# Performance work log

Measured on AMD Instinct MI355X. Metric: run time of the kernel, lower is better.

Reference implementation:

```python
import jax, jax.numpy as jnp
import numpy as np

EPS = 1e-5
DN = ('NCDHW', 'OIDHW', 'NCDHW')

def conv3d(x, w, b):
    y = jax.lax.conv_general_dilated(x, w, (1, 1, 1), 'SAME', dimension_numbers=DN)
    return y + b[None, :, None, None, None]

def batchnorm(x, gamma, beta):
    # training-mode BatchNorm3d: biased batch stats over (N, D, H, W) per channel
    mean = jnp.mean(x, axis=(0, 2, 3, 4), keepdims=True)
    var = jnp.mean((x - mean) ** 2, axis=(0, 2, 3, 4), keepdims=True)
    xhat = (x - mean) * jax.lax.rsqrt(var + EPS)
    return gamma[None, :, None, None, None] * xhat + beta[None, :, None, None, None]

def setup_inputs() -> dict:
    key = jax.random.key(0)
    ks = jax.random.split(key, 8)
    C, N = 32, 4  # channel, fuzzynum
    B, D, H, W = 4, 64, 64, 64
    x = jax.random.normal(ks[0], (B, C, D, H, W), dtype=jnp.float32)
    fan1 = C * 27
    conv1_w = jax.random.uniform(ks[1], (1, C, 3, 3, 3), jnp.float32, -1, 1) / np.sqrt(fan1)
    conv1_b = jnp.zeros((1,), jnp.float32)
    fan2 = 1 * 27
    conv2_w = jax.random.uniform(ks[2], (C, 1, 3, 3, 3), jnp.float32, -1, 1) / np.sqrt(fan2)
    conv2_b = jnp.zeros((C,), jnp.float32)
    mu = jax.random.normal(ks[3], (C, N), dtype=jnp.float32)
    sigma = jax.random.normal(ks[4], (C, N), dtype=jnp.float32)
    bn1_g = jnp.ones((1,), jnp.float32)
    bn1_b = jnp.zeros((1,), jnp.float32)
    bn2_g = jnp.ones((C,), jnp.float32)
    bn2_b = jnp.zeros((C,), jnp.float32)
    return {"x": x, "conv1_w": conv1_w, "conv1_b": conv1_b, "conv2_w": conv2_w,
            "conv2_b": conv2_b, "mu": mu, "sigma": sigma,
            "bn1_g": bn1_g, "bn1_b": bn1_b, "bn2_g": bn2_g, "bn2_b": bn2_b}

def reference(x, conv1_w, conv1_b, conv2_w, conv2_b, mu, sigma, bn1_g, bn1_b, bn2_g, bn2_b):
    x1 = conv3d(x, conv1_w, conv1_b)                      # [B,1,D,H,W]
    # fuzzy Gaussian membership: only channel 0 of mu/sigma is used (x1 has 1 channel)
    m = mu[0]                                             # [n]
    s = sigma[0]                                          # [n]
    z = (x1[..., None] - m) / s                           # [B,1,D,H,W,n]
    fuzz = jnp.exp(-jnp.sum(z * z, axis=-1))              # [B,1,D,H,W]
    y = batchnorm(fuzz, bn1_g, bn1_b)
    y = conv3d(y, conv2_w, conv2_b)                       # [B,C,D,H,W]
    return batchnorm(y, bn2_g, bn2_b)
```

## Files before the change

### kernel.cpp

```cpp
#include <hip/hip_runtime.h>

constexpr int Cc = 32;
constexpr int SP = 64 * 64 * 64;
constexpr int TS = 4 * SP;

constexpr int PW  = 68;
constexpr int PZR = 66 * PW;
constexpr int PSP = 66 * PZR;
constexpr int PTOT = 4 * PSP;

constexpr int WOFF  = 68 + 64 * 64;
constexpr int ACC_N = WOFF + 864;

__global__ __launch_bounds__(256) void k_conv1_fuzzy(
    const float* __restrict__ x, const float* __restrict__ w1,
    const float* __restrict__ b1, const float* __restrict__ mu,
    const float* __restrict__ sg, float* __restrict__ fuzz,
    float* __restrict__ acc)
{
    const int tid = threadIdx.x;
    const int t = blockIdx.x * 256 + tid;
    const int wq = t & 15;        const int w0 = wq << 2;
    const int zp = (t >> 4) & 31; const int z0 = zp << 1;
    const int y  = (t >> 9) & 63;
    const int b  = t >> 15;
    const int lane = tid & 63;

    float S1 = 0.f, S2 = 0.f, S3 = 0.f;
#pragma unroll
    for (int n = 0; n < 4; n++) {
        float m = mu[n], s = sg[n];
        float iv = 1.0f / (s * s);
        S1 += iv; S2 += m * iv; S3 += m * m * iv;
    }

    const float b1v = b1[0];
    float a00 = b1v, a01 = b1v, a02 = b1v, a03 = b1v;
    float a10 = b1v, a11 = b1v, a12 = b1v, a13 = b1v;

    const float* xb = x + (size_t)b * Cc * SP;

    bool pv[12]; int ofs[12];
#pragma unroll
    for (int rz = 0; rz < 4; rz++) {
        const int zz = z0 - 1 + rz;
        const int zzc = min(max(zz, 0), 63);
        const bool okz = (unsigned)zz < 64u;
#pragma unroll
        for (int dy = 0; dy < 3; dy++) {
            const int yy = y - 1 + dy;
            const int yyc = min(max(yy, 0), 63);
            pv[rz * 3 + dy]  = okz && ((unsigned)yy < 64u);
            ofs[rz * 3 + dy] = (zzc << 12) + (yyc << 6) + w0;
        }
    }

    auto LOADCH = [&](int c, float4 (&M)[12]) {
        const float* xc = xb + (size_t)c * SP;
#pragma unroll
        for (int i = 0; i < 12; i++)
            M[i] = *(const float4*)(xc + ofs[i]);
    };

    auto COMPUTECH = [&](int c, float4 (&M)[12]) {
#pragma unroll
        for (int i = 0; i < 12; i++) {
            M[i].x = pv[i] ? M[i].x : 0.f;
            M[i].y = pv[i] ? M[i].y : 0.f;
            M[i].z = pv[i] ? M[i].z : 0.f;
            M[i].w = pv[i] ? M[i].w : 0.f;
        }
        const float* wc = w1 + c * 27;
        float Wv[27];
#pragma unroll
        for (int k = 0; k < 27; k++) Wv[k] = wc[k];
#pragma unroll
        for (int rz = 0; rz < 4; rz++) {
#pragma unroll
            for (int dy = 0; dy < 3; dy++) {
                const float4 m = M[rz * 3 + dy];
                const float lv = __shfl(m.w, (lane + 63) & 63, 64);
                const float rv = __shfl(m.x, (lane + 1) & 63, 64);
                const float v0 = (wq > 0)  ? lv : 0.f;
                const float v5 = (wq < 15) ? rv : 0.f;
                const float v1 = m.x, v2 = m.y, v3 = m.z, v4 = m.w;
                if (rz < 3) {
                    const float W0 = Wv[(rz*3+dy)*3], W1 = Wv[(rz*3+dy)*3+1], W2 = Wv[(rz*3+dy)*3+2];
                    a00 = fmaf(v0, W0, fmaf(v1, W1, fmaf(v2, W2, a00)));
                    a01 = fmaf(v1, W0, fmaf(v2, W1, fmaf(v3, W2, a01)));
                    a02 = fmaf(v2, W0, fmaf(v3, W1, fmaf(v4, W2, a02)));
                    a03 = fmaf(v3, W0, fmaf(v4, W1, fmaf(v5, W2, a03)));
                }
                if (rz >= 1) {
                    const float W0 = Wv[((rz-1)*3+dy)*3], W1 = Wv[((rz-1)*3+dy)*3+1], W2 = Wv[((rz-1)*3+dy)*3+2];
                    a10 = fmaf(v0, W0, fmaf(v1, W1, fmaf(v2, W2, a10)));
                    a11 = fmaf(v1, W0, fmaf(v2, W1, fmaf(v3, W2, a11)));
                    a12 = fmaf(v2, W0, fmaf(v3, W1, fmaf(v4, W2, a12)));
                    a13 = fmaf(v3, W0, fmaf(v4, W1, fmaf(v5, W2, a13)));
                }
            }
        }
    };

    float4 Ma[12], Mb[12];
    LOADCH(0, Ma);
    for (int c = 0; c < Cc; c += 2) {
        LOADCH(c + 1, Mb);
        COMPUTECH(c, Ma);
        if (c + 2 < Cc) LOADCH(c + 2, Ma);
        COMPUTECH(c + 1, Mb);
    }

    float fsum = 0.f, fsq = 0.f;
#pragma unroll
    for (int oz = 0; oz < 2; oz++) {
        float xv[4] = { oz ? a10 : a00, oz ? a11 : a01,
                        oz ? a12 : a02, oz ? a13 : a03 };
        float* fp = fuzz + (size_t)b * PSP + (size_t)(z0 + oz + 1) * PZR
                  + (y + 1) * PW + (w0 + 1);
#pragma unroll
        for (int ow = 0; ow < 4; ow++) {
            float x1 = xv[ow];
            float tt = x1 * x1 * S1 - 2.0f * x1 * S2 + S3;
            float fz = __expf(-tt);
            fp[ow] = fz; fsum += fz; fsq += fz * fz;
        }
    }
#pragma unroll
    for (int m = 1; m < 64; m <<= 1) {
        fsum += __shfl_xor(fsum, m, 64);
        fsq  += __shfl_xor(fsq,  m, 64);
    }
    __shared__ float red[8];
    const int wid = tid >> 6;
    if ((tid & 63) == 0) { red[wid * 2] = fsum; red[wid * 2 + 1] = fsq; }
    __syncthreads();
    if (tid == 0) {
        atomicAdd(&acc[0], red[0] + red[2] + red[4] + red[6]);
        atomicAdd(&acc[1], red[1] + red[3] + red[5] + red[7]);
    }
}

__global__ void k_fin1(const float* __restrict__ g, const float* __restrict__ be,
                       const float* __restrict__ w2, float* __restrict__ acc)
{
    const int tid = threadIdx.x;
    if (tid == 0) {
        float mean = acc[0] * (1.0f / TS);
        float var  = acc[1] * (1.0f / TS) - mean * mean;
        float a = g[0] * rsqrtf(var + 1e-5f);
        acc[2] = a;
        acc[3] = be[0] - mean * a;
    }
    if (tid < 864) {
        const int c   = tid / 27;
        const int cls = tid - c * 27;
        const int zc  = cls / 9;
        const int r   = cls - zc * 9;
        const int yc  = r / 3;
        const int xc  = r - yc * 3;
        float s = 0.f;
#pragma unroll
        for (int dz = 0; dz < 3; dz++) {
            if ((zc == 0 && dz == 0) || (zc == 2 && dz == 2)) continue;
#pragma unroll
            for (int dy = 0; dy < 3; dy++) {
                if ((yc == 0 && dy == 0) || (yc == 2 && dy == 2)) continue;
#pragma unroll
                for (int dx = 0; dx < 3; dx++) {
                    if ((xc == 0 && dx == 0) || (xc == 2 && dx == 2)) continue;
                    s += w2[c * 27 + (dz * 3 + dy) * 3 + dx];
                }
            }
        }
        acc[WOFF + tid] = s;
    }
}

template <bool WRITE>
__global__ __launch_bounds__(256) void k_conv2(
    const float* __restrict__ fuzz, const float* __restrict__ w2,
    const float* __restrict__ b2, float* __restrict__ acc,
    float* __restrict__ out)
{
    const int tid = threadIdx.x;
    const int lane = tid & 63;
    const int wid = __builtin_amdgcn_readfirstlane(tid >> 6);
    const int bi = blockIdx.x;
    const int w = lane;
    const int y = bi & 63;
    const int z0 = ((bi >> 6) & 15) << 2;
    const int b = bi >> 10;
    const float a = acc[2], sh = acc[3];
    const float* fb = fuzz + (size_t)b * PSP;

    float Fl[6][3], Fm[6][3], Fr[6][3];
#pragma unroll
    for (int rz = 0; rz < 6; rz++) {
#pragma unroll
        for (int dy = 0; dy < 3; dy++) {
            const float* rp = fb + (size_t)(z0 + rz) * PZR + (y + dy) * PW + w;
            Fl[rz][dy] = rp[0];
            Fm[rz][dy] = rp[1];
            Fr[rz][dy] = rp[2];
        }
    }

    const int yc  = (y == 0) ? 0 : ((y == 63) ? 2 : 1);
    const int zc0 = (z0 == 0) ? 0 : 1;
    const int zc3 = (z0 + 3 == 63) ? 2 : 1;
    const bool lo = (lane == 0), hi = (lane == 63);

    float* ob = out + (size_t)b * Cc * SP + (z0 << 12) + (y << 6) + w;
    const int slot = bi & 63;
    const int c0 = wid * 8;

#pragma unroll
    for (int ci = 0; ci < 8; ci++) {
        const int c = c0 + ci;
        const float* wc = w2 + c * 27;
        float Wv[27];
#pragma unroll
        for (int k = 0; k < 27; k++) Wv[k] = wc[k];
        float o0 = 0.f, o1 = 0.f, o2 = 0.f, o3 = 0.f;
#pragma unroll
        for (int rz = 0; rz < 6; rz++) {
#pragma unroll
            for (int dy = 0; dy < 3; dy++) {
                const float l = Fl[rz][dy], m = Fm[rz][dy], r = Fr[rz][dy];
#pragma unroll
                for (int oz = 0; oz < 4; oz++) {
                    const int dz = rz - oz;
                    if (dz < 0 || dz > 2) continue;
                    const float W0 = Wv[(dz*3+dy)*3], W1 = Wv[(dz*3+dy)*3+1], W2 = Wv[(dz*3+dy)*3+2];
                    if      (oz == 0) o0 = fmaf(l, W0, fmaf(m, W1, fmaf(r, W2, o0)));
                    else if (oz == 1) o1 = fmaf(l, W0, fmaf(m, W1, fmaf(r, W2, o1)));
                    else if (oz == 2) o2 = fmaf(l, W0, fmaf(m, W1, fmaf(r, W2, o2)));
                    else              o3 = fmaf(l, W0, fmaf(m, W1, fmaf(r, W2, o3)));
                }
            }
        }
        const float bb = b2[c];
        const float* tb = acc + WOFF + c * 27 + yc * 3;
        const float* t0 = tb + zc0 * 9;
        const float* t1 = tb + 9;
        const float* t3 = tb + zc3 * 9;
        const float w0s = lo ? t0[0] : (hi ? t0[2] : t0[1]);
        const float w1s = lo ? t1[0] : (hi ? t1[2] : t1[1]);
        const float w3s = lo ? t3[0] : (hi ? t3[2] : t3[1]);
        const float off0 = fmaf(sh, w0s, bb);
        const float off1 = fmaf(sh, w1s, bb);
        const float off3 = fmaf(sh, w3s, bb);
        const float v0 = fmaf(o0, a, off0);
        const float v1 = fmaf(o1, a, off1);
        const float v2 = fmaf(o2, a, off1);
        const float v3 = fmaf(o3, a, off3);

        if (WRITE) {
            const float sc = acc[4 + c], s2 = acc[36 + c];
            ob[(size_t)c * SP]         = fmaf(v0, sc, s2);
            ob[(size_t)c * SP + 4096]  = fmaf(v1, sc, s2);
            ob[(size_t)c * SP + 8192]  = fmaf(v2, sc, s2);
            ob[(size_t)c * SP + 12288] = fmaf(v3, sc, s2);
        } else {
            float ps = (v0 + v1) + (v2 + v3);
            float pq = fmaf(v0, v0, fmaf(v1, v1, fmaf(v2, v2, v3 * v3)));
#pragma unroll
            for (int mm = 1; mm < 64; mm <<= 1) {
                ps += __shfl_xor(ps, mm, 64);
                pq += __shfl_xor(pq, mm, 64);
            }
            if (lane == 0) {
                atomicAdd(&acc[68 + c * 64 + slot], ps);
                atomicAdd(&acc[68 + (32 + c) * 64 + slot], pq);
            }
        }
    }
}

__global__ void k_fin2(const float* __restrict__ g, const float* __restrict__ be,
                       float* __restrict__ acc)
{
    const int tid = threadIdx.x;
    const int c = tid >> 5, j = tid & 31;
    float s = acc[68 + c * 64 + j]        + acc[68 + c * 64 + 32 + j];
    float q = acc[68 + (32 + c) * 64 + j] + acc[68 + (32 + c) * 64 + 32 + j];
#pragma unroll
    for (int m = 1; m < 32; m <<= 1) {
        s += __shfl_xor(s, m, 32);
        q += __shfl_xor(q, m, 32);
    }
    if (j == 0) {
        float mean = s * (1.0f / TS);
        float var  = q * (1.0f / TS) - mean * mean;
        float sc = g[c] * rsqrtf(var + 1e-5f);
        acc[4 + c]  = sc;
        acc[36 + c] = be[c] - mean * sc;
    }
}

extern "C" void kernel_launch(void* const* d_in, const int* in_sizes, int n_in,
                              void* d_out, int out_size, void* d_ws, size_t ws_size,
                              hipStream_t stream)
{
    const float* x   = (const float*)d_in[0];
    const float* w1  = (const float*)d_in[1];
    const float* b1  = (const float*)d_in[2];
    const float* w2  = (const float*)d_in[3];
    const float* b2  = (const float*)d_in[4];
    const float* mu  = (const float*)d_in[5];
    const float* sg  = (const float*)d_in[6];
    const float* g1  = (const float*)d_in[7];
    const float* be1 = (const float*)d_in[8];
    const float* g2  = (const float*)d_in[9];
    const float* be2 = (const float*)d_in[10];

    float* out  = (float*)d_out;
    float* fuzz = (float*)d_ws;
    float* acc  = fuzz + PTOT;

    hipMemsetAsync(fuzz, 0, (size_t)(PTOT + ACC_N) * sizeof(float), stream);
    k_conv1_fuzzy<<<512, 256, 0, stream>>>(x, w1, b1, mu, sg, fuzz, acc);
    k_fin1<<<1, 864, 0, stream>>>(g1, be1, w2, acc);
    k_conv2<false><<<4096, 256, 0, stream>>>(fuzz, w2, b2, acc, out);
    k_fin2<<<1, 1024, 0, stream>>>(g2, be2, acc);
    k_conv2<true><<<4096, 256, 0, stream>>>(fuzz, w2, b2, acc, out);
}
```

Baseline: 355.3 us.

## Compute one z-plane per conv1 thread and fold BN2 finalize into conv2 write pass

The conv1 kernel now computes one output z-row of four voxels per thread instead of two, which halves the register footprint and doubles the grid. A launch-bounds occupancy hint is added, at the cost of reloading shared z-planes from memory (12 vs 9 rows per output z pair becomes 18). Separately, the k_fin2 kernel is removed and each wave of the writing conv2 pass reduces the per-slot BN2 partial sums itself, saving a launch at the cost of redundant reductions in every block.

```diff
diff --git a/kernel.cpp b/kernel.cpp
--- a/kernel.cpp
+++ b/kernel.cpp
@@ -12,7 +12,7 @@
 constexpr int WOFF  = 68 + 64 * 64;
 constexpr int ACC_N = WOFF + 864;
 
-__global__ __launch_bounds__(256) void k_conv1_fuzzy(
+__global__ __launch_bounds__(256, 4) void k_conv1_fuzzy(
     const float* __restrict__ x, const float* __restrict__ w1,
     const float* __restrict__ b1, const float* __restrict__ mu,
     const float* __restrict__ sg, float* __restrict__ fuzz,
@@ -21,9 +21,9 @@
     const int tid = threadIdx.x;
     const int t = blockIdx.x * 256 + tid;
     const int wq = t & 15;        const int w0 = wq << 2;
-    const int zp = (t >> 4) & 31; const int z0 = zp << 1;
-    const int y  = (t >> 9) & 63;
-    const int b  = t >> 15;
+    const int z  = (t >> 4) & 63;
+    const int y  = (t >> 10) & 63;
+    const int b  = t >> 16;
     const int lane = tid & 63;
 
     float S1 = 0.f, S2 = 0.f, S3 = 0.f;
@@ -35,15 +35,14 @@
     }
 
     const float b1v = b1[0];
-    float a00 = b1v, a01 = b1v, a02 = b1v, a03 = b1v;
-    float a10 = b1v, a11 = b1v, a12 = b1v, a13 = b1v;
+    float a0 = b1v, a1 = b1v, a2 = b1v, a3 = b1v;
 
     const float* xb = x + (size_t)b * Cc * SP;
 
-    bool pv[12]; int ofs[12];
-#pragma unroll
-    for (int rz = 0; rz < 4; rz++) {
-        const int zz = z0 - 1 + rz;
+    bool pv[9]; int ofs[9];
+#pragma unroll
+    for (int rz = 0; rz < 3; rz++) {
+        const int zz = z - 1 + rz;
         const int zzc = min(max(zz, 0), 63);
         const bool okz = (unsigned)zz < 64u;
 #pragma unroll
@@ -55,16 +54,16 @@
         }
     }
 
-    auto LOADCH = [&](int c, float4 (&M)[12]) {
+    auto LOADCH = [&](int c, float4 (&M)[9]) {
         const float* xc = xb + (size_t)c * SP;
 #pragma unroll
-        for (int i = 0; i < 12; i++)
+        for (int i = 0; i < 9; i++)
             M[i] = *(const float4*)(xc + ofs[i]);
     };
 
-    auto COMPUTECH = [&](int c, float4 (&M)[12]) {
-#pragma unroll
-        for (int i = 0; i < 12; i++) {
+    auto COMPUTECH = [&](int c, float4 (&M)[9]) {
+#pragma unroll
+        for (int i = 0; i < 9; i++) {
             M[i].x = pv[i] ? M[i].x : 0.f;
             M[i].y = pv[i] ? M[i].y : 0.f;
             M[i].z = pv[i] ? M[i].z : 0.f;
@@ -75,34 +74,21 @@
 #pragma unroll
         for (int k = 0; k < 27; k++) Wv[k] = wc[k];
 #pragma unroll
-        for (int rz = 0; rz < 4; rz++) {
-#pragma unroll
-            for (int dy = 0; dy < 3; dy++) {
-                const float4 m = M[rz * 3 + dy];
-                const float lv = __shfl(m.w, (lane + 63) & 63, 64);
-                const float rv = __shfl(m.x, (lane + 1) & 63, 64);
-                const float v0 = (wq > 0)  ? lv : 0.f;
-                const float v5 = (wq < 15) ? rv : 0.f;
-                const float v1 = m.x, v2 = m.y, v3 = m.z, v4 = m.w;
-                if (rz < 3) {
-                    const float W0 = Wv[(rz*3+dy)*3], W1 = Wv[(rz*3+dy)*3+1], W2 = Wv[(rz*3+dy)*3+2];
-                    a00 = fmaf(v0, W0, fmaf(v1, W1, fmaf(v2, W2, a00)));
-                    a01 = fmaf(v1, W0, fmaf(v2, W1, fmaf(v3, W2, a01)));
-                    a02 = fmaf(v2, W0, fmaf(v3, W1, fmaf(v4, W2, a02)));
-                    a03 = fmaf(v3, W0, fmaf(v4, W1, fmaf(v5, W2, a03)));
-                }
-                if (rz >= 1) {
-                    const float W0 = Wv[((rz-1)*3+dy)*3], W1 = Wv[((rz-1)*3+dy)*3+1], W2 = Wv[((rz-1)*3+dy)*3+2];
-                    a10 = fmaf(v0, W0, fmaf(v1, W1, fmaf(v2, W2, a10)));
-                    a11 = fmaf(v1, W0, fmaf(v2, W1, fmaf(v3, W2, a11)));
-                    a12 = fmaf(v2, W0, fmaf(v3, W1, fmaf(v4, W2, a12)));
-                    a13 = fmaf(v3, W0, fmaf(v4, W1, fmaf(v5, W2, a13)));
-                }
-            }
+        for (int i = 0; i < 9; i++) {
+            const float4 m = M[i];
+            const float lv = __shfl(m.w, (lane + 63) & 63, 64);
+            const float rv = __shfl(m.x, (lane + 1) & 63, 64);
+            const float v0 = (wq > 0)  ? lv : 0.f;
+            const float v5 = (wq < 15) ? rv : 0.f;
+            const float W0 = Wv[i * 3], W1 = Wv[i * 3 + 1], W2 = Wv[i * 3 + 2];
+            a0 = fmaf(v0,  W0, fmaf(m.x, W1, fmaf(m.y, W2, a0)));
+            a1 = fmaf(m.x, W0, fmaf(m.y, W1, fmaf(m.z, W2, a1)));
+            a2 = fmaf(m.y, W0, fmaf(m.z, W1, fmaf(m.w, W2, a2)));
+            a3 = fmaf(m.z, W0, fmaf(m.w, W1, fmaf(v5,  W2, a3)));
         }
     };
 
-    float4 Ma[12], Mb[12];
+    float4 Ma[9], Mb[9];
     LOADCH(0, Ma);
     for (int c = 0; c < Cc; c += 2) {
         LOADCH(c + 1, Mb);
@@ -112,19 +98,15 @@
     }
 
     float fsum = 0.f, fsq = 0.f;
-#pragma unroll
-    for (int oz = 0; oz < 2; oz++) {
-        float xv[4] = { oz ? a10 : a00, oz ? a11 : a01,
-                        oz ? a12 : a02, oz ? a13 : a03 };
-        float* fp = fuzz + (size_t)b * PSP + (size_t)(z0 + oz + 1) * PZR
-                  + (y + 1) * PW + (w0 + 1);
-#pragma unroll
-        for (int ow = 0; ow < 4; ow++) {
-            float x1 = xv[ow];
-            float tt = x1 * x1 * S1 - 2.0f * x1 * S2 + S3;
-            float fz = __expf(-tt);
-            fp[ow] = fz; fsum += fz; fsq += fz * fz;
-        }
+    float xv[4] = { a0, a1, a2, a3 };
+    float* fp = fuzz + (size_t)b * PSP + (size_t)(z + 1) * PZR
+              + (y + 1) * PW + (w0 + 1);
+#pragma unroll
+    for (int ow = 0; ow < 4; ow++) {
+        float x1 = xv[ow];
+        float tt = x1 * x1 * S1 - 2.0f * x1 * S2 + S3;
+        float fz = __expf(-tt);
+        fp[ow] = fz; fsum += fz; fsq += fz * fz;
     }
 #pragma unroll
     for (int m = 1; m < 64; m <<= 1) {
@@ -180,7 +162,8 @@
 template <bool WRITE>
 __global__ __launch_bounds__(256) void k_conv2(
     const float* __restrict__ fuzz, const float* __restrict__ w2,
-    const float* __restrict__ b2, float* __restrict__ acc,
+    const float* __restrict__ b2, const float* __restrict__ g2,
+    const float* __restrict__ be2, float* __restrict__ acc,
     float* __restrict__ out)
 {
     const int tid = threadIdx.x;
@@ -193,6 +176,27 @@
     const int b = bi >> 10;
     const float a = acc[2], sh = acc[3];
     const float* fb = fuzz + (size_t)b * PSP;
+    const int c0 = wid * 8;
+
+    float scv[8], shv[8];
+    if (WRITE) {
+#pragma unroll
+        for (int ci = 0; ci < 8; ci++) {
+            const int c = c0 + ci;
+            float s = acc[68 + c * 64 + lane];
+            float q = acc[68 + (32 + c) * 64 + lane];
+#pragma unroll
+            for (int mm = 1; mm < 64; mm <<= 1) {
+                s += __shfl_xor(s, mm, 64);
+                q += __shfl_xor(q, mm, 64);
+            }
+            const float mean = s * (1.0f / TS);
+            const float var  = q * (1.0f / TS) - mean * mean;
+            const float sc = g2[c] * rsqrtf(var + 1e-5f);
+            scv[ci] = sc;
+            shv[ci] = be2[c] - mean * sc;
+        }
+    }
 
     float Fl[6][3], Fm[6][3], Fr[6][3];
 #pragma unroll
@@ -213,7 +217,6 @@
 
     float* ob = out + (size_t)b * Cc * SP + (z0 << 12) + (y << 6) + w;
     const int slot = bi & 63;
-    const int c0 = wid * 8;
 
 #pragma unroll
     for (int ci = 0; ci < 8; ci++) {
@@ -257,7 +260,7 @@
         const float v3 = fmaf(o3, a, off3);
 
         if (WRITE) {
-            const float sc = acc[4 + c], s2 = acc[36 + c];
+            const float sc = scv[ci], s2 = shv[ci];
             ob[(size_t)c * SP]         = fmaf(v0, sc, s2);
             ob[(size_t)c * SP + 4096]  = fmaf(v1, sc, s2);
             ob[(size_t)c * SP + 8192]  = fmaf(v2, sc, s2);
@@ -275,27 +278,6 @@
                 atomicAdd(&acc[68 + (32 + c) * 64 + slot], pq);
             }
         }
-    }
-}
-
-__global__ void k_fin2(const float* __restrict__ g, const float* __restrict__ be,
-                       float* __restrict__ acc)
-{
-    const int tid = threadIdx.x;
-    const int c = tid >> 5, j = tid & 31;
-    float s = acc[68 + c * 64 + j]        + acc[68 + c * 64 + 32 + j];
-    float q = acc[68 + (32 + c) * 64 + j] + acc[68 + (32 + c) * 64 + 32 + j];
-#pragma unroll
-    for (int m = 1; m < 32; m <<= 1) {
-        s += __shfl_xor(s, m, 32);
-        q += __shfl_xor(q, m, 32);
-    }
-    if (j == 0) {
-        float mean = s * (1.0f / TS);
-        float var  = q * (1.0f / TS) - mean * mean;
-        float sc = g[c] * rsqrtf(var + 1e-5f);
-        acc[4 + c]  = sc;
-        acc[36 + c] = be[c] - mean * sc;
     }
 }
 
@@ -320,9 +302,8 @@
     float* acc  = fuzz + PTOT;
 
     hipMemsetAsync(fuzz, 0, (size_t)(PTOT + ACC_N) * sizeof(float), stream);
-    k_conv1_fuzzy<<<512, 256, 0, stream>>>(x, w1, b1, mu, sg, fuzz, acc);
+    k_conv1_fuzzy<<<1024, 256, 0, stream>>>(x, w1, b1, mu, sg, fuzz, acc);
     k_fin1<<<1, 864, 0, stream>>>(g1, be1, w2, acc);
-    k_conv2<false><<<4096, 256, 0, stream>>>(fuzz, w2, b2, acc, out);
-    k_fin2<<<1, 1024, 0, stream>>>(g2, be2, acc);
-    k_conv2<true><<<4096, 256, 0, stream>>>(fuzz, w2, b2, acc, out);
+    k_conv2<false><<<4096, 256, 0, stream>>>(fuzz, w2, b2, g2, be2, acc, out);
+    k_conv2<true><<<4096, 256, 0, stream>>>(fuzz, w2, b2, g2, be2, acc, out);
 }
```

After: 536.2 us. 1.51x slower.

## Split conv1 over channel quarters and fuse conv2 with stats, then apply BN2

Applied to the files above, without the earlier changes.

Conv1 is split into four channel groups across 2048 blocks instead of 512, with partial sums written to scratch (reusing the output buffer) and reduced by a new elementwise exp/stats kernel. The conv2 pass now runs once, writing unnormalized output while accumulating BN statistics, and a separate streaming kernel applies the BN2 scale and shift in place. This removes the second conv2 recomputation and adds parallelism to conv1. In exchange it adds extra global traffic for the partial sums and a full read-modify-write of the output. The padded row width grows to 72 so that the new float4 accesses are aligned.

```diff
diff --git a/kernel.cpp b/kernel.cpp
--- a/kernel.cpp
+++ b/kernel.cpp
@@ -4,7 +4,7 @@
 constexpr int SP = 64 * 64 * 64;
 constexpr int TS = 4 * SP;
 
-constexpr int PW  = 68;
+constexpr int PW  = 72;
 constexpr int PZR = 66 * PW;
 constexpr int PSP = 66 * PZR;
 constexpr int PTOT = 4 * PSP;
@@ -12,31 +12,22 @@
 constexpr int WOFF  = 68 + 64 * 64;
 constexpr int ACC_N = WOFF + 864;
 
-__global__ __launch_bounds__(256) void k_conv1_fuzzy(
+__global__ __launch_bounds__(256) void k_conv1_part(
     const float* __restrict__ x, const float* __restrict__ w1,
-    const float* __restrict__ b1, const float* __restrict__ mu,
-    const float* __restrict__ sg, float* __restrict__ fuzz,
-    float* __restrict__ acc)
-{
-    const int tid = threadIdx.x;
-    const int t = blockIdx.x * 256 + tid;
+    float* __restrict__ fuzzA, float* __restrict__ outscratch)
+{
+    const int tid = threadIdx.x;
+    const int bi = blockIdx.x;
+    const int q  = bi >> 9;
+    const int t  = (bi & 511) * 256 + tid;
     const int wq = t & 15;        const int w0 = wq << 2;
     const int zp = (t >> 4) & 31; const int z0 = zp << 1;
     const int y  = (t >> 9) & 63;
     const int b  = t >> 15;
     const int lane = tid & 63;
 
-    float S1 = 0.f, S2 = 0.f, S3 = 0.f;
-#pragma unroll
-    for (int n = 0; n < 4; n++) {
-        float m = mu[n], s = sg[n];
-        float iv = 1.0f / (s * s);
-        S1 += iv; S2 += m * iv; S3 += m * m * iv;
-    }
-
-    const float b1v = b1[0];
-    float a00 = b1v, a01 = b1v, a02 = b1v, a03 = b1v;
-    float a10 = b1v, a11 = b1v, a12 = b1v, a13 = b1v;
+    float a00 = 0.f, a01 = 0.f, a02 = 0.f, a03 = 0.f;
+    float a10 = 0.f, a11 = 0.f, a12 = 0.f, a13 = 0.f;
 
     const float* xb = x + (size_t)b * Cc * SP;
 
@@ -102,30 +93,64 @@
         }
     };
 
+    const int c0 = q * 8;
     float4 Ma[12], Mb[12];
-    LOADCH(0, Ma);
-    for (int c = 0; c < Cc; c += 2) {
+    LOADCH(c0, Ma);
+    for (int c = c0; c < c0 + 8; c += 2) {
         LOADCH(c + 1, Mb);
         COMPUTECH(c, Ma);
-        if (c + 2 < Cc) LOADCH(c + 2, Ma);
+        if (c + 2 < c0 + 8) LOADCH(c + 2, Ma);
         COMPUTECH(c + 1, Mb);
     }
 
+    float* dst = (q == 0) ? fuzzA : (outscratch + (size_t)(q - 1) * PTOT);
+    float* fp0 = dst + (size_t)b * PSP + (size_t)(z0 + 1) * PZR + (y + 1) * PW + 4 + w0;
+    *(float4*)fp0         = make_float4(a00, a01, a02, a03);
+    *(float4*)(fp0 + PZR) = make_float4(a10, a11, a12, a13);
+}
+
+__global__ __launch_bounds__(256) void k_fuzzy_exp(
+    float* __restrict__ fuzzA, const float* __restrict__ outscratch,
+    const float* __restrict__ b1, const float* __restrict__ mu,
+    const float* __restrict__ sg, float* __restrict__ acc)
+{
+    const int tid = threadIdx.x;
+    const int t = blockIdx.x * 256 + tid;
+    const int wq = t & 15;
+    const int z  = (t >> 4) & 63;
+    const int y  = (t >> 10) & 63;
+    const int b  = t >> 16;
+
+    float S1 = 0.f, S2 = 0.f, S3 = 0.f;
+#pragma unroll
+    for (int n = 0; n < 4; n++) {
+        float m = mu[n], s = sg[n];
+        float iv = 1.0f / (s * s);
+        S1 += iv; S2 += m * iv; S3 += m * m * iv;
+    }
+    const float b1v = b1[0];
+
+    const size_t idx = (size_t)b * PSP + (size_t)(z + 1) * PZR + (y + 1) * PW + 4 + (wq << 2);
+    float4 s0 = *(const float4*)(fuzzA + idx);
+    float4 s1 = *(const float4*)(outscratch + idx);
+    float4 s2 = *(const float4*)(outscratch + PTOT + idx);
+    float4 s3 = *(const float4*)(outscratch + 2 * (size_t)PTOT + idx);
+
+    float xs[4] = { s0.x + s1.x + s2.x + s3.x + b1v,
+                    s0.y + s1.y + s2.y + s3.y + b1v,
+                    s0.z + s1.z + s2.z + s3.z + b1v,
+                    s0.w + s1.w + s2.w + s3.w + b1v };
+    float4 fv; float* fp = &fv.x;
     float fsum = 0.f, fsq = 0.f;
 #pragma unroll
-    for (int oz = 0; oz < 2; oz++) {
-        float xv[4] = { oz ? a10 : a00, oz ? a11 : a01,
-                        oz ? a12 : a02, oz ? a13 : a03 };
-        float* fp = fuzz + (size_t)b * PSP + (size_t)(z0 + oz + 1) * PZR
-                  + (y + 1) * PW + (w0 + 1);
-#pragma unroll
-        for (int ow = 0; ow < 4; ow++) {
-            float x1 = xv[ow];
-            float tt = x1 * x1 * S1 - 2.0f * x1 * S2 + S3;
-            float fz = __expf(-tt);
-            fp[ow] = fz; fsum += fz; fsq += fz * fz;
-        }
-    }
+    for (int ow = 0; ow < 4; ow++) {
+        const float x1 = xs[ow];
+        const float tt = x1 * x1 * S1 - 2.0f * x1 * S2 + S3;
+        const float fz = __expf(-tt);
+        fp[ow] = fz; fsum += fz; fsq += fz * fz;
+    }
+    *(float4*)(fuzzA + idx) = fv;
+
 #pragma unroll
     for (int m = 1; m < 64; m <<= 1) {
         fsum += __shfl_xor(fsum, m, 64);
@@ -177,8 +202,7 @@
     }
 }
 
-template <bool WRITE>
-__global__ __launch_bounds__(256) void k_conv2(
+__global__ __launch_bounds__(256) void k_conv2_fused(
     const float* __restrict__ fuzz, const float* __restrict__ w2,
     const float* __restrict__ b2, float* __restrict__ acc,
     float* __restrict__ out)
@@ -193,13 +217,14 @@
     const int b = bi >> 10;
     const float a = acc[2], sh = acc[3];
     const float* fb = fuzz + (size_t)b * PSP;
+    const int c0 = wid * 8;
 
     float Fl[6][3], Fm[6][3], Fr[6][3];
 #pragma unroll
     for (int rz = 0; rz < 6; rz++) {
 #pragma unroll
         for (int dy = 0; dy < 3; dy++) {
-            const float* rp = fb + (size_t)(z0 + rz) * PZR + (y + dy) * PW + w;
+            const float* rp = fb + (size_t)(z0 + rz) * PZR + (y + dy) * PW + w + 3;
             Fl[rz][dy] = rp[0];
             Fm[rz][dy] = rp[1];
             Fr[rz][dy] = rp[2];
@@ -213,7 +238,6 @@
 
     float* ob = out + (size_t)b * Cc * SP + (z0 << 12) + (y << 6) + w;
     const int slot = bi & 63;
-    const int c0 = wid * 8;
 
 #pragma unroll
     for (int ci = 0; ci < 8; ci++) {
@@ -256,47 +280,57 @@
         const float v2 = fmaf(o2, a, off1);
         const float v3 = fmaf(o3, a, off3);
 
-        if (WRITE) {
-            const float sc = acc[4 + c], s2 = acc[36 + c];
-            ob[(size_t)c * SP]         = fmaf(v0, sc, s2);
-            ob[(size_t)c * SP + 4096]  = fmaf(v1, sc, s2);
-            ob[(size_t)c * SP + 8192]  = fmaf(v2, sc, s2);
-            ob[(size_t)c * SP + 12288] = fmaf(v3, sc, s2);
-        } else {
-            float ps = (v0 + v1) + (v2 + v3);
-            float pq = fmaf(v0, v0, fmaf(v1, v1, fmaf(v2, v2, v3 * v3)));
-#pragma unroll
-            for (int mm = 1; mm < 64; mm <<= 1) {
-                ps += __shfl_xor(ps, mm, 64);
-                pq += __shfl_xor(pq, mm, 64);
-            }
-            if (lane == 0) {
-                atomicAdd(&acc[68 + c * 64 + slot], ps);
-                atomicAdd(&acc[68 + (32 + c) * 64 + slot], pq);
-            }
-        }
-    }
-}
-
-__global__ void k_fin2(const float* __restrict__ g, const float* __restrict__ be,
-                       float* __restrict__ acc)
-{
-    const int tid = threadIdx.x;
-    const int c = tid >> 5, j = tid & 31;
-    float s = acc[68 + c * 64 + j]        + acc[68 + c * 64 + 32 + j];
-    float q = acc[68 + (32 + c) * 64 + j] + acc[68 + (32 + c) * 64 + 32 + j];
-#pragma unroll
-    for (int m = 1; m < 32; m <<= 1) {
-        s += __shfl_xor(s, m, 32);
-        q += __shfl_xor(q, m, 32);
-    }
-    if (j == 0) {
-        float mean = s * (1.0f / TS);
-        float var  = q * (1.0f / TS) - mean * mean;
-        float sc = g[c] * rsqrtf(var + 1e-5f);
-        acc[4 + c]  = sc;
-        acc[36 + c] = be[c] - mean * sc;
-    }
+        ob[(size_t)c * SP]         = v0;
+        ob[(size_t)c * SP + 4096]  = v1;
+        ob[(size_t)c * SP + 8192]  = v2;
+        ob[(size_t)c * SP + 12288] = v3;
+
+        float ps = (v0 + v1) + (v2 + v3);
+        float pq = fmaf(v0, v0, fmaf(v1, v1, fmaf(v2, v2, v3 * v3)));
+#pragma unroll
+        for (int mm = 1; mm < 64; mm <<= 1) {
+            ps += __shfl_xor(ps, mm, 64);
+            pq += __shfl_xor(pq, mm, 64);
+        }
+        if (lane == 0) {
+            atomicAdd(&acc[68 + c * 64 + slot], ps);
+            atomicAdd(&acc[68 + (32 + c) * 64 + slot], pq);
+        }
+    }
+}
+
+__global__ __launch_bounds__(256) void k_bn2_apply(
+    const float* __restrict__ g2, const float* __restrict__ be2,
+    const float* __restrict__ acc, float* __restrict__ out)
+{
+    const int tid = threadIdx.x;
+    const int t = blockIdx.x * 256 + tid;
+    const int c = (t >> 16) & 31;
+    __shared__ float bc[2];
+    if (tid < 64) {
+        float s = acc[68 + c * 64 + tid];
+        float q = acc[68 + (32 + c) * 64 + tid];
+#pragma unroll
+        for (int mm = 1; mm < 64; mm <<= 1) {
+            s += __shfl_xor(s, mm, 64);
+            q += __shfl_xor(q, mm, 64);
+        }
+        if (tid == 0) {
+            const float mean = s * (1.0f / TS);
+            const float var  = q * (1.0f / TS) - mean * mean;
+            const float sc = g2[c] * rsqrtf(var + 1e-5f);
+            bc[0] = sc;
+            bc[1] = be2[c] - mean * sc;
+        }
+    }
+    __syncthreads();
+    const float sc = bc[0], shf = bc[1];
+    float4 v = ((const float4*)out)[t];
+    v.x = fmaf(v.x, sc, shf);
+    v.y = fmaf(v.y, sc, shf);
+    v.z = fmaf(v.z, sc, shf);
+    v.w = fmaf(v.w, sc, shf);
+    ((float4*)out)[t] = v;
 }
 
 extern "C" void kernel_launch(void* const* d_in, const int* in_sizes, int n_in,
@@ -320,9 +354,9 @@
     float* acc  = fuzz + PTOT;
 
     hipMemsetAsync(fuzz, 0, (size_t)(PTOT + ACC_N) * sizeof(float), stream);
-    k_conv1_fuzzy<<<512, 256, 0, stream>>>(x, w1, b1, mu, sg, fuzz, acc);
+    k_conv1_part<<<2048, 256, 0, stream>>>(x, w1, fuzz, out);
+    k_fuzzy_exp<<<1024, 256, 0, stream>>>(fuzz, out, b1, mu, sg, acc);
     k_fin1<<<1, 864, 0, stream>>>(g1, be1, w2, acc);
-    k_conv2<false><<<4096, 256, 0, stream>>>(fuzz, w2, b2, acc, out);
-    k_fin2<<<1, 1024, 0, stream>>>(g2, be2, acc);
-    k_conv2<true><<<4096, 256, 0, stream>>>(fuzz, w2, b2, acc, out);
-}
+    k_conv2_fused<<<4096, 256, 0, stream>>>(fuzz, w2, b2, acc, out);
+    k_bn2_apply<<<32768, 256, 0, stream>>>(g2, be2, acc, out);
+}
```

Result: slower. 395.4 us (+11.3%).
